# Performance work log

Measured on AMD Instinct MI355X. Metric: run time of the kernel, lower is better.

The kernel has to match this reference:

```python
import jax, jax.numpy as jnp
import numpy as np

N = 8192
F_IN = 512
F_OUT = 64
ALPHA = 0.2  # LeakyReLU negative slope
MASK_VAL = -9e15


def setup_inputs() -> dict:
    key = jax.random.key(0)
    k1, k2, k3, k4, k5 = jax.random.split(key, 5)
    x = jax.random.normal(k1, (N, F_IN), dtype=jnp.float32)
    adj = jax.random.randint(k2, (N, N), 0, 2, dtype=jnp.int32)
    # params: W uniform(-stdv, stdv) per reset_parameters, A xavier-ish
    stdv = 1.0 / np.sqrt(F_OUT)
    W = jax.random.uniform(k3, (F_IN, F_OUT), dtype=jnp.float32, minval=-stdv, maxval=stdv)
    bias = jax.random.uniform(k4, (F_OUT,), dtype=jnp.float32, minval=-stdv, maxval=stdv)
    A = jax.random.normal(k5, (2 * F_OUT, 1), dtype=jnp.float32) * 0.1
    return {"x": x, "adj": adj, "W": W, "bias": bias, "A": A}


def reference(x, adj, W, bias, A):
    # Wh: [N, F_OUT]
    Wh = x @ W
    # e_ij = leakyrelu([Wh_i || Wh_j] @ A) == leakyrelu(Wh_i @ a1 + Wh_j @ a2)
    # (mathematically identical to the N x N x 2F concat, without materializing it)
    a1 = A[:F_OUT, 0]  # [F_OUT]
    a2 = A[F_OUT:, 0]  # [F_OUT]
    s1 = Wh @ a1  # [N]
    s2 = Wh @ a2  # [N]
    e = jax.nn.leaky_relu(s1[:, None] + s2[None, :], negative_slope=ALPHA)  # [N, N]
    masked = jnp.where(adj > 0, e, MASK_VAL)
    attention = jax.nn.softmax(masked, axis=1)  # [N, N]
    # dropout p=0.0 -> identity
    out = attention @ Wh + bias  # [N, F_OUT]
    return out
```

## Files before the change

### kernel.cpp

```cpp
#include <hip/hip_runtime.h>

#define NN 8192
#define FIN 512
#define FOUT 64
#define LRELU_ALPHA 0.2f
#define LOG2E 1.4426950408889634f

typedef __attribute__((ext_vector_type(4))) float f32x4;
typedef __attribute__((ext_vector_type(4))) int i32x4;
typedef __attribute__((ext_vector_type(8))) __bf16 bf16x8;

#if __has_builtin(__builtin_amdgcn_exp2f)
#define EXP2F(x) __builtin_amdgcn_exp2f(x)
#else
#define EXP2F(x) exp2f(x)
#endif

__global__ __launch_bounds__(256) void gat_wh(
    const float* __restrict__ x, const float* __restrict__ W,
    const float* __restrict__ A,
    __bf16* __restrict__ Wpk, float* __restrict__ s1, float* __restrict__ s2)
{
    const int wid  = (blockIdx.x * 256 + threadIdx.x) >> 6;
    const int lane = threadIdx.x & 63;
    const int cg   = lane & 15;
    const int kh   = lane >> 4;
    const int row0 = wid * 4;

    f32x4 acc[4];
    #pragma unroll
    for (int r_ = 0; r_ < 4; ++r_) acc[r_] = (f32x4){0.f, 0.f, 0.f, 0.f};

    const float* xb   = x + (size_t)row0 * FIN + kh * 128;
    const float* wcol = W + cg * 4 + (size_t)kh * 128 * FOUT;

    #pragma unroll 2
    for (int k = 0; k < 128; k += 4) {
        f32x4 wv[4];
        #pragma unroll
        for (int u = 0; u < 4; ++u)
            wv[u] = *reinterpret_cast<const f32x4*>(wcol + (size_t)(k + u) * FOUT);
        #pragma unroll
        for (int r_ = 0; r_ < 4; ++r_) {
            f32x4 xv = *reinterpret_cast<const f32x4*>(xb + (size_t)r_ * FIN + k);
            acc[r_] += xv[0] * wv[0];
            acc[r_] += xv[1] * wv[1];
            acc[r_] += xv[2] * wv[2];
            acc[r_] += xv[3] * wv[3];
        }
    }

    #pragma unroll
    for (int r_ = 0; r_ < 4; ++r_) {
        #pragma unroll
        for (int u = 0; u < 4; ++u) {
            acc[r_][u] += __shfl_xor(acc[r_][u], 16);
            acc[r_][u] += __shfl_xor(acc[r_][u], 32);
        }
    }

    f32x4 a1v = *reinterpret_cast<const f32x4*>(A + cg * 4);
    f32x4 a2v = *reinterpret_cast<const f32x4*>(A + FOUT + cg * 4);
    #pragma unroll
    for (int r_ = 0; r_ < 4; ++r_) {
        float s1p = acc[r_][0]*a1v[0] + acc[r_][1]*a1v[1] + acc[r_][2]*a1v[2] + acc[r_][3]*a1v[3];
        float s2p = acc[r_][0]*a2v[0] + acc[r_][1]*a2v[1] + acc[r_][2]*a2v[2] + acc[r_][3]*a2v[3];
        #pragma unroll
        for (int off = 1; off < 16; off <<= 1) {
            s1p += __shfl_xor(s1p, off);
            s2p += __shfl_xor(s2p, off);
        }
        if (lane == 0) { s1[row0 + r_] = s1p; s2[row0 + r_] = s2p; }
    }

    {
        const int fb = cg >> 2;
        const int rr = ((cg & 3) << 2) + kh;
        #pragma unroll
        for (int r_ = 0; r_ < 4; ++r_) {
            const int node = row0 + r_;
            const int c    = node >> 5;
            const int qq   = (node >> 3) & 3;
            const int j    = node & 7;
            Wpk[((size_t)((c << 2) + fb) << 9) + (qq << 7) + (rr << 3) + j]
                = (__bf16)acc[r_][kh];
        }
    }
}

__global__ __launch_bounds__(256) void gat_attn(
    const int* __restrict__ adj, const __bf16* __restrict__ Wpk,
    const float* __restrict__ s1g, const float* __restrict__ s2g,
    const float* __restrict__ bias, float* __restrict__ out)
{
    __shared__ float s2l[NN];
    __shared__ float red[4];
    __shared__ float ol[4][16];
    __shared__ float oacc[4][16][FOUT];

    const int tid  = threadIdx.x;
    const int w    = tid >> 6;
    const int lane = tid & 63;
    const int r    = lane & 15;
    const int q    = lane >> 4;
    const int row0 = blockIdx.x * 16;

    float mx = -3.0e38f;
    for (int i = tid; i < NN / 4; i += 256) {
        f32x4 v = reinterpret_cast<const f32x4*>(s2g)[i];
        v *= LOG2E;
        reinterpret_cast<f32x4*>(s2l)[i] = v;
        mx = fmaxf(mx, fmaxf(fmaxf(v[0], v[1]), fmaxf(v[2], v[3])));
    }
    #pragma unroll
    for (int off = 1; off < 64; off <<= 1)
        mx = fmaxf(mx, __shfl_xor(mx, off));
    if (lane == 0) red[w] = mx;
    __syncthreads();
    const float s2maxl = fmaxf(fmaxf(red[0], red[1]), fmaxf(red[2], red[3]));

    const float s1l = s1g[row0 + r] * LOG2E;
    const float tM  = s1l + s2maxl;
    const float Ml  = fmaxf(tM, LRELU_ALPHA * tM);
    const float c1  = s1l - Ml;
    const float c2  = LRELU_ALPHA * s1l - Ml;

    const __bf16 oneb = (__bf16)1.0f;
    const bf16x8 onesv = {oneb, oneb, oneb, oneb, oneb, oneb, oneb, oneb};

    f32x4 acc0 = {0,0,0,0}, acc1 = {0,0,0,0}, acc2 = {0,0,0,0}, acc3 = {0,0,0,0};
    f32x4 accL = {0,0,0,0};

    const int*    adjp = adj + (size_t)(row0 + r) * NN + (w << 11) + (q << 3);
    const __bf16* wq   = Wpk + ((size_t)w << 17) + ((size_t)lane << 3);
    const float*  s2p_ = s2l + (w << 11) + (q << 3);

    for (int it = 0; it < 32; ++it) {
        const int j0 = it << 6;
        #pragma unroll
        for (int c = 0; c < 2; ++c) {
            const int jc = j0 + (c << 5);
            const __bf16* ph = wq + ((size_t)(jc >> 5) << 11);
            i32x4 av0 = *reinterpret_cast<const i32x4*>(adjp + jc);
            i32x4 av1 = *reinterpret_cast<const i32x4*>(adjp + jc + 4);
            bf16x8 b0 = *reinterpret_cast<const bf16x8*>(ph);
            bf16x8 b1 = *reinterpret_cast<const bf16x8*>(ph + 512);
            bf16x8 b2 = *reinterpret_cast<const bf16x8*>(ph + 1024);
            bf16x8 b3 = *reinterpret_cast<const bf16x8*>(ph + 1536);
            f32x4 s2a = *reinterpret_cast<const f32x4*>(s2p_ + jc);
            f32x4 s2c = *reinterpret_cast<const f32x4*>(s2p_ + jc + 4);

            bf16x8 af;
            #pragma unroll
            for (int i = 0; i < 4; ++i) {
                float g0 = fmaxf(c1 + s2a[i], fmaf(LRELU_ALPHA, s2a[i], c2));
                g0 = (av0[i] > 0) ? g0 : -3.0e38f;
                af[i] = (__bf16)EXP2F(g0);
                float g1 = fmaxf(c1 + s2c[i], fmaf(LRELU_ALPHA, s2c[i], c2));
                g1 = (av1[i] > 0) ? g1 : -3.0e38f;
                af[i + 4] = (__bf16)EXP2F(g1);
            }
            acc0 = __builtin_amdgcn_mfma_f32_16x16x32_bf16(af, b0, acc0, 0, 0, 0);
            acc1 = __builtin_amdgcn_mfma_f32_16x16x32_bf16(af, b1, acc1, 0, 0, 0);
            acc2 = __builtin_amdgcn_mfma_f32_16x16x32_bf16(af, b2, acc2, 0, 0, 0);
            acc3 = __builtin_amdgcn_mfma_f32_16x16x32_bf16(af, b3, acc3, 0, 0, 0);
            accL = __builtin_amdgcn_mfma_f32_16x16x32_bf16(af, onesv, accL, 0, 0, 0);
        }
    }

    if (r == 0) {
        #pragma unroll
        for (int reg = 0; reg < 4; ++reg) ol[w][(q << 2) + reg] = accL[reg];
    }
    #pragma unroll
    for (int reg = 0; reg < 4; ++reg) {
        oacc[w][(q << 2) + reg][0 * 16 + r] = acc0[reg];
        oacc[w][(q << 2) + reg][1 * 16 + r] = acc1[reg];
        oacc[w][(q << 2) + reg][2 * 16 + r] = acc2[reg];
        oacc[w][(q << 2) + reg][3 * 16 + r] = acc3[reg];
    }
    __syncthreads();

    for (int o = tid; o < 16 * FOUT; o += 256) {
        const int rr = o >> 6;
        const int f  = o & 63;
        const float L = ol[0][rr] + ol[1][rr] + ol[2][rr] + ol[3][rr];
        const float O = oacc[0][rr][f] + oacc[1][rr][f] + oacc[2][rr][f] + oacc[3][rr][f];
        out[(size_t)(row0 + rr) * FOUT + f] = O / L + bias[f];
    }
}

extern "C" void kernel_launch(void* const* d_in, const int* in_sizes, int n_in,
                              void* d_out, int out_size, void* d_ws, size_t ws_size,
                              hipStream_t stream)
{
    const float* x    = (const float*)d_in[0];
    const int*   adj  = (const int*)d_in[1];
    const float* W    = (const float*)d_in[2];
    const float* bias = (const float*)d_in[3];
    const float* A    = (const float*)d_in[4];
    float* out = (float*)d_out;

    char* ws = (char*)d_ws;
    __bf16* Wpk = (__bf16*)ws;
    float*  s1  = (float*)(ws + (size_t)FOUT * NN * sizeof(__bf16));
    float*  s2  = s1 + NN;

    gat_wh<<<dim3(512), dim3(256), 0, stream>>>(x, W, A, Wpk, s1, s2);
    gat_attn<<<dim3(NN / 16), dim3(256), 0, stream>>>(adj, Wpk, s1, s2, bias, out);
}
```

Before: 405.4 us.

## Process two 16-row tiles per wave in attention kernel with 512-thread blocks

The attention kernel now handles 32 rows per block with 8 waves. Each wave computes two 16-row MFMA tiles over a 1024-column slice, reusing each loaded Wh fragment and s2 value for both tiles. This halves Wh fragment loads and s2 staging per row and adds instruction-level parallelism. In exchange it uses more registers and shared memory (larger oacc buffer) and launches half as many blocks, which may reduce occupancy and latency hiding.

```diff
diff --git a/kernel.cpp b/kernel.cpp
--- a/kernel.cpp
+++ b/kernel.cpp
@@ -88,25 +88,25 @@
     }
 }
 
-__global__ __launch_bounds__(256) void gat_attn(
+__global__ __launch_bounds__(512) void gat_attn(
     const int* __restrict__ adj, const __bf16* __restrict__ Wpk,
     const float* __restrict__ s1g, const float* __restrict__ s2g,
     const float* __restrict__ bias, float* __restrict__ out)
 {
     __shared__ float s2l[NN];
-    __shared__ float red[4];
-    __shared__ float ol[4][16];
-    __shared__ float oacc[4][16][FOUT];
+    __shared__ float red[8];
+    __shared__ float ol[8][32];
+    __shared__ float oacc[8][32][FOUT];
 
     const int tid  = threadIdx.x;
     const int w    = tid >> 6;
     const int lane = tid & 63;
     const int r    = lane & 15;
     const int q    = lane >> 4;
-    const int row0 = blockIdx.x * 16;
+    const int row0 = blockIdx.x * 32;
 
     float mx = -3.0e38f;
-    for (int i = tid; i < NN / 4; i += 256) {
+    for (int i = tid; i < NN / 4; i += 512) {
         f32x4 v = reinterpret_cast<const f32x4*>(s2g)[i];
         v *= LOG2E;
         reinterpret_cast<f32x4*>(s2l)[i] = v;
@@ -117,75 +117,103 @@
         mx = fmaxf(mx, __shfl_xor(mx, off));
     if (lane == 0) red[w] = mx;
     __syncthreads();
-    const float s2maxl = fmaxf(fmaxf(red[0], red[1]), fmaxf(red[2], red[3]));
-
-    const float s1l = s1g[row0 + r] * LOG2E;
-    const float tM  = s1l + s2maxl;
-    const float Ml  = fmaxf(tM, LRELU_ALPHA * tM);
-    const float c1  = s1l - Ml;
-    const float c2  = LRELU_ALPHA * s1l - Ml;
+    float s2maxl = red[0];
+    #pragma unroll
+    for (int i = 1; i < 8; ++i) s2maxl = fmaxf(s2maxl, red[i]);
+
+    const float s1A = s1g[row0 + r] * LOG2E;
+    const float s1B = s1g[row0 + 16 + r] * LOG2E;
+    const float tMA = s1A + s2maxl;
+    const float tMB = s1B + s2maxl;
+    const float MlA = fmaxf(tMA, LRELU_ALPHA * tMA);
+    const float MlB = fmaxf(tMB, LRELU_ALPHA * tMB);
+    const float c1A = s1A - MlA, c2A = LRELU_ALPHA * s1A - MlA;
+    const float c1B = s1B - MlB, c2B = LRELU_ALPHA * s1B - MlB;
 
     const __bf16 oneb = (__bf16)1.0f;
     const bf16x8 onesv = {oneb, oneb, oneb, oneb, oneb, oneb, oneb, oneb};
 
-    f32x4 acc0 = {0,0,0,0}, acc1 = {0,0,0,0}, acc2 = {0,0,0,0}, acc3 = {0,0,0,0};
-    f32x4 accL = {0,0,0,0};
-
-    const int*    adjp = adj + (size_t)(row0 + r) * NN + (w << 11) + (q << 3);
-    const __bf16* wq   = Wpk + ((size_t)w << 17) + ((size_t)lane << 3);
-    const float*  s2p_ = s2l + (w << 11) + (q << 3);
-
-    for (int it = 0; it < 32; ++it) {
-        const int j0 = it << 6;
-        #pragma unroll
-        for (int c = 0; c < 2; ++c) {
-            const int jc = j0 + (c << 5);
-            const __bf16* ph = wq + ((size_t)(jc >> 5) << 11);
-            i32x4 av0 = *reinterpret_cast<const i32x4*>(adjp + jc);
-            i32x4 av1 = *reinterpret_cast<const i32x4*>(adjp + jc + 4);
-            bf16x8 b0 = *reinterpret_cast<const bf16x8*>(ph);
-            bf16x8 b1 = *reinterpret_cast<const bf16x8*>(ph + 512);
-            bf16x8 b2 = *reinterpret_cast<const bf16x8*>(ph + 1024);
-            bf16x8 b3 = *reinterpret_cast<const bf16x8*>(ph + 1536);
-            f32x4 s2a = *reinterpret_cast<const f32x4*>(s2p_ + jc);
-            f32x4 s2c = *reinterpret_cast<const f32x4*>(s2p_ + jc + 4);
-
-            bf16x8 af;
-            #pragma unroll
-            for (int i = 0; i < 4; ++i) {
-                float g0 = fmaxf(c1 + s2a[i], fmaf(LRELU_ALPHA, s2a[i], c2));
-                g0 = (av0[i] > 0) ? g0 : -3.0e38f;
-                af[i] = (__bf16)EXP2F(g0);
-                float g1 = fmaxf(c1 + s2c[i], fmaf(LRELU_ALPHA, s2c[i], c2));
-                g1 = (av1[i] > 0) ? g1 : -3.0e38f;
-                af[i + 4] = (__bf16)EXP2F(g1);
-            }
-            acc0 = __builtin_amdgcn_mfma_f32_16x16x32_bf16(af, b0, acc0, 0, 0, 0);
-            acc1 = __builtin_amdgcn_mfma_f32_16x16x32_bf16(af, b1, acc1, 0, 0, 0);
-            acc2 = __builtin_amdgcn_mfma_f32_16x16x32_bf16(af, b2, acc2, 0, 0, 0);
-            acc3 = __builtin_amdgcn_mfma_f32_16x16x32_bf16(af, b3, acc3, 0, 0, 0);
-            accL = __builtin_amdgcn_mfma_f32_16x16x32_bf16(af, onesv, accL, 0, 0, 0);
-        }
+    f32x4 accA0 = {0,0,0,0}, accA1 = {0,0,0,0}, accA2 = {0,0,0,0}, accA3 = {0,0,0,0};
+    f32x4 accB0 = {0,0,0,0}, accB1 = {0,0,0,0}, accB2 = {0,0,0,0}, accB3 = {0,0,0,0};
+    f32x4 accLA = {0,0,0,0}, accLB = {0,0,0,0};
+
+    const int*    adjpA = adj + (size_t)(row0 + r) * NN + (w << 10) + (q << 3);
+    const int*    adjpB = adjpA + (size_t)16 * NN;
+    const __bf16* wq    = Wpk + ((size_t)w << 16) + ((size_t)lane << 3);
+    const float*  s2p_  = s2l + (w << 10) + (q << 3);
+
+    for (int h = 0; h < 32; ++h) {
+        const int jc = h << 5;
+        const __bf16* ph = wq + ((size_t)h << 11);
+
+        i32x4 avA0 = *reinterpret_cast<const i32x4*>(adjpA + jc);
+        i32x4 avA1 = *reinterpret_cast<const i32x4*>(adjpA + jc + 4);
+        i32x4 avB0 = *reinterpret_cast<const i32x4*>(adjpB + jc);
+        i32x4 avB1 = *reinterpret_cast<const i32x4*>(adjpB + jc + 4);
+        bf16x8 b0 = *reinterpret_cast<const bf16x8*>(ph);
+        bf16x8 b1 = *reinterpret_cast<const bf16x8*>(ph + 512);
+        bf16x8 b2 = *reinterpret_cast<const bf16x8*>(ph + 1024);
+        bf16x8 b3 = *reinterpret_cast<const bf16x8*>(ph + 1536);
+        f32x4 s2a = *reinterpret_cast<const f32x4*>(s2p_ + jc);
+        f32x4 s2c = *reinterpret_cast<const f32x4*>(s2p_ + jc + 4);
+
+        bf16x8 afA, afB;
+        #pragma unroll
+        for (int i = 0; i < 4; ++i) {
+            float gA0 = fmaxf(c1A + s2a[i], fmaf(LRELU_ALPHA, s2a[i], c2A));
+            gA0 = (avA0[i] > 0) ? gA0 : -3.0e38f;
+            afA[i] = (__bf16)EXP2F(gA0);
+            float gA1 = fmaxf(c1A + s2c[i], fmaf(LRELU_ALPHA, s2c[i], c2A));
+            gA1 = (avA1[i] > 0) ? gA1 : -3.0e38f;
+            afA[i + 4] = (__bf16)EXP2F(gA1);
+            float gB0 = fmaxf(c1B + s2a[i], fmaf(LRELU_ALPHA, s2a[i], c2B));
+            gB0 = (avB0[i] > 0) ? gB0 : -3.0e38f;
+            afB[i] = (__bf16)EXP2F(gB0);
+            float gB1 = fmaxf(c1B + s2c[i], fmaf(LRELU_ALPHA, s2c[i], c2B));
+            gB1 = (avB1[i] > 0) ? gB1 : -3.0e38f;
+            afB[i + 4] = (__bf16)EXP2F(gB1);
+        }
+        accA0 = __builtin_amdgcn_mfma_f32_16x16x32_bf16(afA, b0, accA0, 0, 0, 0);
+        accA1 = __builtin_amdgcn_mfma_f32_16x16x32_bf16(afA, b1, accA1, 0, 0, 0);
+        accA2 = __builtin_amdgcn_mfma_f32_16x16x32_bf16(afA, b2, accA2, 0, 0, 0);
+        accA3 = __builtin_amdgcn_mfma_f32_16x16x32_bf16(afA, b3, accA3, 0, 0, 0);
+        accLA = __builtin_amdgcn_mfma_f32_16x16x32_bf16(afA, onesv, accLA, 0, 0, 0);
+        accB0 = __builtin_amdgcn_mfma_f32_16x16x32_bf16(afB, b0, accB0, 0, 0, 0);
+        accB1 = __builtin_amdgcn_mfma_f32_16x16x32_bf16(afB, b1, accB1, 0, 0, 0);
+        accB2 = __builtin_amdgcn_mfma_f32_16x16x32_bf16(afB, b2, accB2, 0, 0, 0);
+        accB3 = __builtin_amdgcn_mfma_f32_16x16x32_bf16(afB, b3, accB3, 0, 0, 0);
+        accLB = __builtin_amdgcn_mfma_f32_16x16x32_bf16(afB, onesv, accLB, 0, 0, 0);
     }
 
     if (r == 0) {
         #pragma unroll
-        for (int reg = 0; reg < 4; ++reg) ol[w][(q << 2) + reg] = accL[reg];
+        for (int reg = 0; reg < 4; ++reg) {
+            ol[w][(q << 2) + reg]      = accLA[reg];
+            ol[w][16 + (q << 2) + reg] = accLB[reg];
+        }
     }
     #pragma unroll
     for (int reg = 0; reg < 4; ++reg) {
-        oacc[w][(q << 2) + reg][0 * 16 + r] = acc0[reg];
-        oacc[w][(q << 2) + reg][1 * 16 + r] = acc1[reg];
-        oacc[w][(q << 2) + reg][2 * 16 + r] = acc2[reg];
-        oacc[w][(q << 2) + reg][3 * 16 + r] = acc3[reg];
+        oacc[w][(q << 2) + reg][0 * 16 + r] = accA0[reg];
+        oacc[w][(q << 2) + reg][1 * 16 + r] = accA1[reg];
+        oacc[w][(q << 2) + reg][2 * 16 + r] = accA2[reg];
+        oacc[w][(q << 2) + reg][3 * 16 + r] = accA3[reg];
+        oacc[w][16 + (q << 2) + reg][0 * 16 + r] = accB0[reg];
+        oacc[w][16 + (q << 2) + reg][1 * 16 + r] = accB1[reg];
+        oacc[w][16 + (q << 2) + reg][2 * 16 + r] = accB2[reg];
+        oacc[w][16 + (q << 2) + reg][3 * 16 + r] = accB3[reg];
     }
     __syncthreads();
 
-    for (int o = tid; o < 16 * FOUT; o += 256) {
+    for (int o = tid; o < 32 * FOUT; o += 512) {
         const int rr = o >> 6;
         const int f  = o & 63;
-        const float L = ol[0][rr] + ol[1][rr] + ol[2][rr] + ol[3][rr];
-        const float O = oacc[0][rr][f] + oacc[1][rr][f] + oacc[2][rr][f] + oacc[3][rr][f];
+        float L = 0.f, O = 0.f;
+        #pragma unroll
+        for (int w2 = 0; w2 < 8; ++w2) {
+            L += ol[w2][rr];
+            O += oacc[w2][rr][f];
+        }
         out[(size_t)(row0 + rr) * FOUT + f] = O / L + bias[f];
     }
 }
@@ -207,5 +235,5 @@
     float*  s2  = s1 + NN;
 
     gat_wh<<<dim3(512), dim3(256), 0, stream>>>(x, W, A, Wpk, s1, s2);
-    gat_attn<<<dim3(NN / 16), dim3(256), 0, stream>>>(adj, Wpk, s1, s2, bias, out);
+    gat_attn<<<dim3(NN / 32), dim3(512), 0, stream>>>(adj, Wpk, s1, s2, bias, out);
 }
```

Result: slower. 418.7 us (+3.3%).
